# Kernel tuning notes

Hardware: AMD Instinct MI355X
Metric: run time of the kernel (lower is better)

Reference implementation:

```python
import jax, jax.numpy as jnp
import numpy as np

V, D, H, L, FF, NC = 32000, 512, 8, 4, 2048, 10
HD = D // H
EPS = 1e-5


def _layernorm(x, g, b):
    m = jnp.mean(x, axis=-1, keepdims=True)
    v = jnp.mean((x - m) ** 2, axis=-1, keepdims=True)
    return (x - m) * jax.lax.rsqrt(v + EPS) * g + b


def _pos_encoding(T, d):
    pos = jnp.arange(T, dtype=jnp.float32)[:, None]
    div = jnp.exp(jnp.arange(0, d, 2, dtype=jnp.float32) * (-np.log(10000.0) / d))
    pe = jnp.zeros((T, d), dtype=jnp.float32)
    pe = pe.at[:, 0::2].set(jnp.sin(pos * div))
    pe = pe.at[:, 1::2].set(jnp.cos(pos * div))
    return pe


def setup_inputs() -> dict:
    key = jax.random.key(0)
    ks = iter(jax.random.split(key, 32))
    n = lambda shape, s=0.02: jax.random.normal(next(ks), shape, dtype=jnp.float32) * s
    inp = {
        "tokens": jax.random.randint(next(ks), (8, 1024), 0, V),
        "emb": n((V, D), 1.0),
        # attention projections, stored (in, out) so y = x @ W + b
        "Wq": n((L, D, D)), "bq": jnp.zeros((L, D)),
        "Wk": n((L, D, D)), "bk": jnp.zeros((L, D)),
        "Wv": n((L, D, D)), "bv": jnp.zeros((L, D)),
        "Wo": n((L, D, D)), "bo": jnp.zeros((L, D)),
        "ln1_g": jnp.ones((L, D)), "ln1_b": jnp.zeros((L, D)),
        "ln2_g": jnp.ones((L, D)), "ln2_b": jnp.zeros((L, D)),
        "W1": n((L, D, FF)), "b1": jnp.zeros((L, FF)),
        "W2": n((L, FF, D)), "b2": jnp.zeros((L, D)),
        "heavy_w": n((D, D)), "heavy_b": jnp.zeros((D,)),
        "heavy_a1": n((D, D)), "heavy_a2": n((D, D)),
        "norm_g": jnp.ones((D,)), "norm_b": jnp.zeros((D,)),
        "cls_W": n((D, NC)), "cls_b": jnp.zeros((NC,)),
    }
    return inp


def reference(tokens, emb, Wq, bq, Wk, bk, Wv, bv, Wo, bo,
              ln1_g, ln1_b, ln2_g, ln2_b, W1, b1, W2, b2,
              heavy_w, heavy_b, heavy_a1, heavy_a2,
              norm_g, norm_b, cls_W, cls_b):
    B, T = tokens.shape
    x = emb[tokens] + _pos_encoding(T, D)[None]  # [B,T,D]
    scale = 1.0 / np.sqrt(HD)
    for l in range(L):
        # attention block (pre-norm)
        h = _layernorm(x, ln1_g[l], ln1_b[l])
        q = (h @ Wq[l] + bq[l]).reshape(B, T, H, HD)
        k = (h @ Wk[l] + bk[l]).reshape(B, T, H, HD)
        v = (h @ Wv[l] + bv[l]).reshape(B, T, H, HD)
        scores = jnp.einsum("bqhd,bkhd->bhqk", q, k) * scale
        attn = jax.nn.softmax(scores, axis=-1)
        o = jnp.einsum("bhqk,bkhd->bqhd", attn, v).reshape(B, T, D)
        x = x + (o @ Wo[l] + bo[l])
        # feedforward block
        h = _layernorm(x, ln2_g[l], ln2_b[l])
        x = x + (jax.nn.gelu(h @ W1[l] + b1[l], approximate=False) @ W2[l] + b2[l])
    # heavy layer: chained matmuls + bias + tanh (vectorized over B*T)
    x = jnp.tanh(((x @ heavy_w) @ heavy_a1) @ heavy_a2 + heavy_b)
    x = _layernorm(x, norm_g, norm_b)
    x = jnp.mean(x, axis=1)  # [B,D]
    return x @ cls_W + cls_b  # [B,NC]
```

## Files before the change

### kernel.cpp

```cpp
#include <hip/hip_runtime.h>
#include <math.h>

#define BS   8
#define TT   1024
#define DD   512
#define HH   8
#define LL   4
#define FFD  2048
#define NCC  10
#define MM   (BS*TT)
#define MDl  ((long)MM*DD)

typedef unsigned short u16;
typedef short  short8 __attribute__((ext_vector_type(8)));
typedef float  f32x4  __attribute__((ext_vector_type(4)));
typedef u16    u16x8  __attribute__((ext_vector_type(8)));
typedef u16    u16x4  __attribute__((ext_vector_type(4)));

static __device__ __forceinline__ u16 f2b(float f) {
    union { float f; unsigned u; } x; x.f = f;
    unsigned r = x.u + 0x7FFFu + ((x.u >> 16) & 1u);
    return (u16)(r >> 16);
}
static __device__ __forceinline__ u16 f2b_fast(float f) {
    union { float f; unsigned u; } x; x.f = f;
    return (u16)((x.u + 0x8000u) >> 16);
}
static __device__ __forceinline__ float b2f(u16 u) {
    union { unsigned u; float f; } x; x.u = ((unsigned)u) << 16;
    return x.f;
}

__global__ __launch_bounds__(256)
void embed_kernel(const int* __restrict__ tok, const float* __restrict__ emb,
                  float* __restrict__ X) {
    int i = blockIdx.x * 256 + threadIdx.x;
    int d = i & (DD - 1);
    int row = i >> 9;
    int t = row & (TT - 1);
    int j = d >> 1;
    float freq = __expf((float)(2 * j) * (-9.210340371976184f / 512.0f));
    float ang = (float)t * freq;
    float pe = (d & 1) ? cosf(ang) : sinf(ang);
    X[i] = emb[(long)tok[row] * DD + d] + pe;
}

template<int OUTBF>
__global__ __launch_bounds__(256)
void ln_kernel(const float* __restrict__ in, void* __restrict__ outp,
               const float* __restrict__ g, const float* __restrict__ b) {
    int row = blockIdx.x;
    int tid = threadIdx.x;
    const float* x = in + (long)row * DD;
    float x1 = x[tid], x2 = x[tid + 256];
    __shared__ float red[256], red2[256];
    red[tid] = x1 + x2;
    red2[tid] = x1 * x1 + x2 * x2;
    __syncthreads();
    for (int st = 128; st > 0; st >>= 1) {
        if (tid < st) { red[tid] += red[tid + st]; red2[tid] += red2[tid + st]; }
        __syncthreads();
    }
    float mean = red[0] * (1.0f / DD);
    float var = red2[0] * (1.0f / DD) - mean * mean;
    float rstd = rsqrtf(var + 1e-5f);
    float y1 = (x1 - mean) * rstd * g[tid] + b[tid];
    float y2 = (x2 - mean) * rstd * g[tid + 256] + b[tid + 256];
    if (OUTBF) {
        u16* o = (u16*)outp + (long)row * DD;
        o[tid] = f2b(y1); o[tid + 256] = f2b(y2);
    } else {
        float* o = (float*)outp + (long)row * DD;
        o[tid] = y1; o[tid + 256] = y2;
    }
}

template<int OUTBF, int HAS_BIAS, int ACT, int HAS_RES>
__global__ __launch_bounds__(512, 2)
void mfma_gemm(const u16* __restrict__ A, const u16* __restrict__ BT,
               const float* __restrict__ bias, const float* __restrict__ R,
               void* __restrict__ Cout, int N, int K) {
    __shared__ __align__(16) u16 lds[17408];
    u16* As = lds;
    u16* Bs = lds + 8192;
    const int tid = threadIdx.x;
    const int lane = tid & 63;
    const int w = tid >> 6;
    const int wm = w >> 1;
    const int wn = w & 1;
    const long bm = (long)blockIdx.y * 128;
    const long bn = (long)blockIdx.x * 128;

    f32x4 acc[2][4];
#pragma unroll
    for (int i = 0; i < 2; ++i)
#pragma unroll
        for (int j = 0; j < 4; ++j) acc[i][j] = {0.f, 0.f, 0.f, 0.f};

    const int srow = tid >> 2;
    const int sc0 = (tid & 3) * 2;
    const u16* Ag = A + (bm + srow) * K + sc0 * 8;
    const u16* Bg = BT + (bn + srow) * K + sc0 * 8;
    int soff[2];
#pragma unroll
    for (int j = 0; j < 2; ++j)
        soff[j] = srow * 64 + ((sc0 + j) ^ (srow & 7)) * 8;

    const int fr = lane & 15;
    const int g = lane >> 4;
    const int am0 = wm * 32 + fr;
    const int bn0 = wn * 64 + fr;
    const int sw = fr & 7;

    u16x8 sa[2][2], sb[2][2];
#pragma unroll
    for (int j = 0; j < 2; ++j) {
        sa[0][j] = *(const u16x8*)(Ag + j * 8);
        sb[0][j] = *(const u16x8*)(Bg + j * 8);
    }

    for (int k0 = 0; k0 < K; k0 += 128) {
#pragma unroll
        for (int half = 0; half < 2; ++half) {
            const int cb = half, nb = half ^ 1;
            __syncthreads();
#pragma unroll
            for (int j = 0; j < 2; ++j) {
                *(u16x8*)&As[soff[j]] = sa[cb][j];
                *(u16x8*)&Bs[soff[j]] = sb[cb][j];
            }
            const int knext = k0 + (half + 1) * 64;
            if (knext < K) {
#pragma unroll
                for (int j = 0; j < 2; ++j) {
                    sa[nb][j] = *(const u16x8*)(Ag + knext + j * 8);
                    sb[nb][j] = *(const u16x8*)(Bg + knext + j * 8);
                }
            }
            __syncthreads();
#pragma unroll
            for (int kk = 0; kk < 2; ++kk) {
                const int pos = ((kk << 2) + g) ^ sw;
                short8 af[2], bfv[4];
#pragma unroll
                for (int mi = 0; mi < 2; ++mi)
                    af[mi] = *(const short8*)&As[(am0 + mi * 16) * 64 + pos * 8];
#pragma unroll
                for (int ni = 0; ni < 4; ++ni)
                    bfv[ni] = *(const short8*)&Bs[(bn0 + ni * 16) * 64 + pos * 8];
#pragma unroll
                for (int mi = 0; mi < 2; ++mi)
#pragma unroll
                    for (int ni = 0; ni < 4; ++ni)
                        acc[mi][ni] = __builtin_amdgcn_mfma_f32_16x16x32_bf16(
                            af[mi], bfv[ni], acc[mi][ni], 0, 0, 0);
            }
        }
    }

    const int erow0 = wm * 32 + g * 4;
    const int ecol0 = wn * 64 + fr;

    if (OUTBF) {
        __syncthreads();
#pragma unroll
        for (int ni = 0; ni < 4; ++ni) {
            const long col = bn + ecol0 + ni * 16;
            float bv = 0.f;
            if (HAS_BIAS) bv = bias[col];
#pragma unroll
            for (int mi = 0; mi < 2; ++mi)
#pragma unroll
                for (int r = 0; r < 4; ++r) {
                    const int row = erow0 + mi * 16 + r;
                    float v = acc[mi][ni][r];
                    if (HAS_BIAS) v += bv;
                    if (ACT == 1) v = 0.5f * v * (1.0f + erff(v * 0.70710678118654752f));
                    if (ACT == 2) v = tanhf(v);
                    if (HAS_RES) v += R[(bm + row) * N + col];
                    lds[row * 136 + ecol0 + ni * 16] = f2b(v);
                }
        }
        __syncthreads();
        const int srow2 = tid >> 4;
        const int sch2 = tid & 15;
        u16* Cp = (u16*)Cout;
#pragma unroll
        for (int rr = 0; rr < 4; ++rr) {
            const int row = srow2 + rr * 32;
            u16x8 vv = *(const u16x8*)&lds[row * 136 + sch2 * 8];
            *(u16x8*)(Cp + (bm + row) * N + bn + sch2 * 8) = vv;
        }
    } else {
#pragma unroll
        for (int ni = 0; ni < 4; ++ni) {
            const long col = bn + ecol0 + ni * 16;
            float bv = 0.f;
            if (HAS_BIAS) bv = bias[col];
#pragma unroll
            for (int mi = 0; mi < 2; ++mi)
#pragma unroll
                for (int r = 0; r < 4; ++r) {
                    const long row = bm + erow0 + mi * 16 + r;
                    float v = acc[mi][ni][r];
                    if (HAS_BIAS) v += bv;
                    if (ACT == 1) v = 0.5f * v * (1.0f + erff(v * 0.70710678118654752f));
                    if (ACT == 2) v = tanhf(v);
                    if (HAS_RES) v += R[row * N + col];
                    ((float*)Cout)[row * N + col] = v;
                }
        }
    }
}

__global__ __launch_bounds__(256, 2)
void attn_kernel(const u16* __restrict__ QKV, u16* __restrict__ O) {
    const int qblk = blockIdx.x;
    const int h = blockIdx.y;
    const int b = blockIdx.z;
    const int tid = threadIdx.x;
    const int lane = tid & 63;
    const int w = tid >> 6;
    const int fr = lane & 15;
    const int g = lane >> 4;
    const int q8 = g * 8;

    __shared__ __align__(16) u16 Ks[64 * 64];
    __shared__ __align__(16) u16 Vt[64 * 72];
    __shared__ __align__(16) u16 Pw[4][32 * 72];

    const long rowb = (long)b * TT;
    const int wq0 = qblk * 128 + w * 32;

    short8 qf[2][2];
#pragma unroll
    for (int qt = 0; qt < 2; ++qt)
#pragma unroll
        for (int hf = 0; hf < 2; ++hf)
            qf[qt][hf] = *(const short8*)(QKV + (rowb + wq0 + qt * 16 + fr) * 1536
                                          + h * 64 + hf * 32 + q8);

    f32x4 accO[2][4];
    float lsum[2][4];
#pragma unroll
    for (int qt = 0; qt < 2; ++qt) {
#pragma unroll
        for (int nt = 0; nt < 4; ++nt) accO[qt][nt] = {0.f, 0.f, 0.f, 0.f};
#pragma unroll
        for (int r = 0; r < 4; ++r) lsum[qt][r] = 0.f;
    }

    const int skey = tid >> 2;
    const int skc = (tid & 3) * 2;
    const int koff0 = skey * 64 + ((skc ^ (skey & 7)) * 8);
    const int koff1 = skey * 64 + (((skc + 1) ^ (skey & 7)) * 8);
    const int vkp = tid & 31;
    const int vd0 = (tid >> 5) * 8;

    auto load_kv = [&](int kt_, u16x8* kr_, u16x8* vr_) {
        const long tb_ = (rowb + (long)kt_ * 64) * 1536 + h * 64;
        const u16* kp_ = QKV + tb_ + 512 + (long)skey * 1536 + skc * 8;
        kr_[0] = *(const u16x8*)kp_;
        kr_[1] = *(const u16x8*)(kp_ + 8);
        const u16* vp_ = QKV + tb_ + 1024 + (long)(vkp * 2) * 1536 + vd0;
        vr_[0] = *(const u16x8*)vp_;
        vr_[1] = *(const u16x8*)(vp_ + 1536);
    };
    auto stage = [&](u16x8* kr_, u16x8* vr_) {
        *(u16x8*)&Ks[koff0] = kr_[0];
        *(u16x8*)&Ks[koff1] = kr_[1];
        unsigned* Vt32 = (unsigned*)Vt;
#pragma unroll
        for (int j = 0; j < 8; ++j)
            Vt32[(vd0 + j) * 36 + vkp] =
                (unsigned)vr_[0][j] | ((unsigned)vr_[1][j] << 16);
    };
    auto compute = [&]() {
        f32x4 accS[2][4];
#pragma unroll
        for (int qt = 0; qt < 2; ++qt)
#pragma unroll
            for (int n = 0; n < 4; ++n) accS[qt][n] = {0.f, 0.f, 0.f, 0.f};
#pragma unroll
        for (int n = 0; n < 4; ++n)
#pragma unroll
            for (int hf = 0; hf < 2; ++hf) {
                short8 bk = *(const short8*)&Ks[(n * 16 + fr) * 64
                                                + ((((hf << 2) + g) ^ (fr & 7)) * 8)];
                accS[0][n] = __builtin_amdgcn_mfma_f32_16x16x32_bf16(qf[0][hf], bk, accS[0][n], 0, 0, 0);
                accS[1][n] = __builtin_amdgcn_mfma_f32_16x16x32_bf16(qf[1][hf], bk, accS[1][n], 0, 0, 0);
            }
#pragma unroll
        for (int qt = 0; qt < 2; ++qt)
#pragma unroll
            for (int r = 0; r < 4; ++r) {
                int prow = qt * 16 + g * 4 + r;
#pragma unroll
                for (int n = 0; n < 4; ++n) {
                    float pv = exp2f(accS[qt][n][r] * 0.18033688011112042f);
                    lsum[qt][r] += pv;
                    Pw[w][prow * 72 + n * 16 + fr] = f2b_fast(pv);
                }
            }
#pragma unroll
        for (int hf = 0; hf < 2; ++hf) {
            short8 pa0 = *(const short8*)&Pw[w][fr * 72 + hf * 32 + q8];
            short8 pa1 = *(const short8*)&Pw[w][(16 + fr) * 72 + hf * 32 + q8];
#pragma unroll
            for (int nt = 0; nt < 4; ++nt) {
                short8 bv = *(const short8*)&Vt[(nt * 16 + fr) * 72 + hf * 32 + q8];
                accO[0][nt] = __builtin_amdgcn_mfma_f32_16x16x32_bf16(pa0, bv, accO[0][nt], 0, 0, 0);
                accO[1][nt] = __builtin_amdgcn_mfma_f32_16x16x32_bf16(pa1, bv, accO[1][nt], 0, 0, 0);
            }
        }
    };

    u16x8 krA[2], vrA[2], krB[2], vrB[2];
    load_kv(0, krA, vrA);

#pragma unroll 1
    for (int kt = 0; kt < 16; kt += 2) {
        __syncthreads();
        stage(krA, vrA);
        load_kv(kt + 1, krB, vrB);
        __syncthreads();
        compute();
        __syncthreads();
        stage(krB, vrB);
        if (kt + 2 < 16) load_kv(kt + 2, krA, vrA);
        __syncthreads();
        compute();
    }

#pragma unroll
    for (int qt = 0; qt < 2; ++qt)
#pragma unroll
        for (int r = 0; r < 4; ++r) {
            float s = lsum[qt][r];
            s += __shfl_xor(s, 1, 64);
            s += __shfl_xor(s, 2, 64);
            s += __shfl_xor(s, 4, 64);
            s += __shfl_xor(s, 8, 64);
            lsum[qt][r] = 1.0f / s;
        }
#pragma unroll
    for (int qt = 0; qt < 2; ++qt)
#pragma unroll
        for (int nt = 0; nt < 4; ++nt)
#pragma unroll
            for (int r = 0; r < 4; ++r) {
                long row = rowb + wq0 + qt * 16 + g * 4 + r;
                O[row * DD + h * 64 + nt * 16 + fr] = f2b(accO[qt][nt][r] * lsum[qt][r]);
            }
}

struct WP   { const float* s; u16* d; };
struct WTbl { WP e[19]; };

__global__ __launch_bounds__(256)
void wprep512_kernel(WTbl tbl) {
    const float* src = tbl.e[blockIdx.z].s;
    u16* dst = tbl.e[blockIdx.z].d;
    int k0 = blockIdx.y * 32, n0 = blockIdx.x * 32;
    __shared__ float tile[32][33];
    int tx = threadIdx.x & 31, ty = threadIdx.x >> 5;
#pragma unroll
    for (int i = 0; i < 4; ++i)
        tile[ty + 8 * i][tx] = src[(long)(k0 + ty + 8 * i) * 512 + n0 + tx];
    __syncthreads();
#pragma unroll
    for (int i = 0; i < 4; ++i) {
        int r = ty + 8 * i;
        dst[(long)(n0 + r) * 512 + k0 + tx] = f2b(tile[tx][r]);
    }
}

__global__ __launch_bounds__(256)
void wprep_kernel(const float* __restrict__ src, u16* __restrict__ dst,
                  int K, int N, long srcLS, long dstLS) {
    int l = blockIdx.z;
    src += (long)l * srcLS;
    dst += (long)l * dstLS;
    int k0 = blockIdx.y * 32, n0 = blockIdx.x * 32;
    __shared__ float tile[32][33];
    int tx = threadIdx.x & 31, ty = threadIdx.x >> 5;
#pragma unroll
    for (int i = 0; i < 4; ++i)
        tile[ty + 8 * i][tx] = src[(long)(k0 + ty + 8 * i) * N + n0 + tx];
    __syncthreads();
#pragma unroll
    for (int i = 0; i < 4; ++i) {
        int r = ty + 8 * i;
        dst[(long)(n0 + r) * K + k0 + tx] = f2b(tile[tx][r]);
    }
}

__global__ __launch_bounds__(256)
void bprep_kernel(const float* __restrict__ bq, const float* __restrict__ bk,
                  const float* __restrict__ bv, float* __restrict__ dst) {
    int i = blockIdx.x * 256 + threadIdx.x;
    int l = i / 1536, j = i - l * 1536;
    float v = (j < 512) ? bq[l * 512 + j]
            : (j < 1024) ? bk[l * 512 + j - 512]
                         : bv[l * 512 + j - 1024];
    dst[i] = v;
}

__global__ __launch_bounds__(256)
void f2b_kernel(const float* __restrict__ in, u16* __restrict__ out, int n) {
    int i = blockIdx.x * 256 + threadIdx.x;
    if (i < n) out[i] = f2b(in[i]);
}

__global__ __launch_bounds__(256)
void zero_kernel(float* __restrict__ p, int n) {
    int i = blockIdx.x * 256 + threadIdx.x;
    if (i < n) p[i] = 0.0f;
}

__global__ __launch_bounds__(256)
void colmean_kernel(const float* __restrict__ Hn, float* __restrict__ XM) {
    int blk = blockIdx.x;
    int b = blk >> 5;
    int r0 = (blk & 31) * 32;
    int tid = threadIdx.x;
    float acc0 = 0.0f, acc1 = 0.0f;
    for (int r = 0; r < 32; ++r) {
        long off = ((long)b * TT + r0 + r) * DD + tid;
        acc0 += Hn[off];
        acc1 += Hn[off + 256];
    }
    atomicAdd(&XM[b * DD + tid], acc0);
    atomicAdd(&XM[b * DD + tid + 256], acc1);
}

__global__ __launch_bounds__(256)
void cls_kernel(const float* __restrict__ XM, const float* __restrict__ W,
                const float* __restrict__ bias, float* __restrict__ out) {
    int b = blockIdx.x;
    int tid = threadIdx.x;
    __shared__ float xm[DD];
    xm[tid] = XM[b * DD + tid] * (1.0f / TT);
    xm[tid + 256] = XM[b * DD + tid + 256] * (1.0f / TT);
    __syncthreads();
    if (tid < NCC) {
        float s = bias[tid];
        for (int d = 0; d < DD; ++d) s += xm[d] * W[d * NCC + tid];
        out[b * NCC + tid] = s;
    }
}

extern "C" void kernel_launch(void* const* d_in, const int* in_sizes, int n_in,
                              void* d_out, int out_size, void* d_ws, size_t ws_size,
                              hipStream_t stream) {
    const int*   tokens  = (const int*)d_in[0];
    const float* emb     = (const float*)d_in[1];
    const float* Wq      = (const float*)d_in[2];
    const float* bq      = (const float*)d_in[3];
    const float* Wk      = (const float*)d_in[4];
    const float* bk      = (const float*)d_in[5];
    const float* Wv      = (const float*)d_in[6];
    const float* bv      = (const float*)d_in[7];
    const float* Wo      = (const float*)d_in[8];
    const float* bo      = (const float*)d_in[9];
    const float* ln1_g   = (const float*)d_in[10];
    const float* ln1_b   = (const float*)d_in[11];
    const float* ln2_g   = (const float*)d_in[12];
    const float* ln2_b   = (const float*)d_in[13];
    const float* W1      = (const float*)d_in[14];
    const float* b1      = (const float*)d_in[15];
    const float* W2      = (const float*)d_in[16];
    const float* b2      = (const float*)d_in[17];
    const float* heavy_w = (const float*)d_in[18];
    const float* heavy_b = (const float*)d_in[19];
    const float* heavy_a1= (const float*)d_in[20];
    const float* heavy_a2= (const float*)d_in[21];
    const float* norm_g  = (const float*)d_in[22];
    const float* norm_b  = (const float*)d_in[23];
    const float* cls_W   = (const float*)d_in[24];
    const float* cls_b   = (const float*)d_in[25];
    float* out = (float*)d_out;

    char* p = (char*)d_ws;
    float* X    = (float*)p;  p += MDl * 4;
    u16*   Hh   = (u16*)p;    p += MDl * 2;
    u16*   QKVb = (u16*)p;
    u16*   FFb  = QKVb;
    u16*   T1   = QKVb;
    u16*   T2   = QKVb + MDl;
    float* LNout= (float*)QKVb;
    p += (long)MM * 1536 * 2;
    u16*   Ob   = (u16*)p;    p += MDl * 2;
    u16*   Xbf  = (u16*)p;    p += MDl * 2;
    u16*   WqkvT= (u16*)p;    p += 4L * 1536 * 512 * 2;
    u16*   WoT  = (u16*)p;    p += 4L * 512 * 512 * 2;
    u16*   W1T  = (u16*)p;    p += 4L * 2048 * 512 * 2;
    u16*   W2T  = (u16*)p;    p += 4L * 512 * 2048 * 2;
    u16*   WhT  = (u16*)p;    p += 3L * 512 * 512 * 2;
    float* bqkv = (float*)p;  p += 4L * 1536 * 4;
    float* XM   = (float*)p;  p += (long)BS * DD * 4;

    dim3 blk(256);
    dim3 blk512(512);

    WTbl tbl;
    for (int l = 0; l < 4; ++l) {
        tbl.e[l * 4 + 0] = {Wq + (long)l * 262144, WqkvT + (long)l * 786432};
        tbl.e[l * 4 + 1] = {Wk + (long)l * 262144, WqkvT + (long)l * 786432 + 262144};
        tbl.e[l * 4 + 2] = {Wv + (long)l * 262144, WqkvT + (long)l * 786432 + 524288};
        tbl.e[l * 4 + 3] = {Wo + (long)l * 262144, WoT + (long)l * 262144};
    }
    tbl.e[16] = {heavy_w,  WhT};
    tbl.e[17] = {heavy_a1, WhT + 262144};
    tbl.e[18] = {heavy_a2, WhT + 524288};
    wprep512_kernel<<<dim3(16, 16, 19), blk, 0, stream>>>(tbl);
    wprep_kernel<<<dim3(64, 16, 4), blk, 0, stream>>>(W1, W1T,  512, 2048, 1048576, 1048576);
    wprep_kernel<<<dim3(16, 64, 4), blk, 0, stream>>>(W2, W2T, 2048,  512, 1048576, 1048576);
    bprep_kernel<<<24, blk, 0, stream>>>(bq, bk, bv, bqkv);

    embed_kernel<<<MM * DD / 256, blk, 0, stream>>>(tokens, emb, X);

    dim3 gQKV(12, 64), g512(4, 64), gFF1(16, 64);

    for (int l = 0; l < LL; ++l) {
        ln_kernel<1><<<MM, blk, 0, stream>>>(X, Hh, ln1_g + l * DD, ln1_b + l * DD);
        mfma_gemm<1, 1, 0, 0><<<gQKV, blk512, 0, stream>>>(
            Hh, WqkvT + (long)l * 786432, bqkv + l * 1536, nullptr, QKVb, 1536, 512);
        attn_kernel<<<dim3(8, HH, BS), blk, 0, stream>>>(QKVb, Ob);
        mfma_gemm<0, 1, 0, 1><<<g512, blk512, 0, stream>>>(
            Ob, WoT + (long)l * 262144, bo + l * DD, X, X, 512, 512);
        ln_kernel<1><<<MM, blk, 0, stream>>>(X, Hh, ln2_g + l * DD, ln2_b + l * DD);
        mfma_gemm<1, 1, 1, 0><<<gFF1, blk512, 0, stream>>>(
            Hh, W1T + (long)l * 1048576, b1 + l * FFD, nullptr, FFb, 2048, 512);
        mfma_gemm<0, 1, 0, 1><<<g512, blk512, 0, stream>>>(
            FFb, W2T + (long)l * 1048576, b2 + l * DD, X, X, 512, 2048);
    }

    f2b_kernel<<<MM * DD / 256, blk, 0, stream>>>(X, Xbf, MM * DD);
    mfma_gemm<1, 0, 0, 0><<<g512, blk512, 0, stream>>>(Xbf, WhT,          nullptr, nullptr, T1, 512, 512);
    mfma_gemm<1, 0, 0, 0><<<g512, blk512, 0, stream>>>(T1,  WhT + 262144, nullptr, nullptr, T2, 512, 512);
    mfma_gemm<0, 1, 2, 0><<<g512, blk512, 0, stream>>>(T2,  WhT + 524288, heavy_b, nullptr, X,  512, 512);

    ln_kernel<0><<<MM, blk, 0, stream>>>(X, LNout, norm_g, norm_b);
    zero_kernel<<<(BS * DD + 255) / 256, blk, 0, stream>>>(XM, BS * DD);
    colmean_kernel<<<256, blk, 0, stream>>>(LNout, XM);
    cls_kernel<<<BS, blk, 0, stream>>>(XM, cls_W, cls_b, out);
}
```

Before: 829.5 us.

## Keep residual stream in bf16 and restructure GEMM k-loop double buffering

```diff
diff --git a/kernel.cpp b/kernel.cpp
--- a/kernel.cpp
+++ b/kernel.cpp
@@ -33,7 +33,7 @@
 
 __global__ __launch_bounds__(256)
 void embed_kernel(const int* __restrict__ tok, const float* __restrict__ emb,
-                  float* __restrict__ X) {
+                  u16* __restrict__ X) {
     int i = blockIdx.x * 256 + threadIdx.x;
     int d = i & (DD - 1);
     int row = i >> 9;
@@ -42,17 +42,23 @@
     float freq = __expf((float)(2 * j) * (-9.210340371976184f / 512.0f));
     float ang = (float)t * freq;
     float pe = (d & 1) ? cosf(ang) : sinf(ang);
-    X[i] = emb[(long)tok[row] * DD + d] + pe;
-}
-
-template<int OUTBF>
-__global__ __launch_bounds__(256)
-void ln_kernel(const float* __restrict__ in, void* __restrict__ outp,
+    X[i] = f2b(emb[(long)tok[row] * DD + d] + pe);
+}
+
+template<int INBF, int OUTBF>
+__global__ __launch_bounds__(256)
+void ln_kernel(const void* __restrict__ inp, void* __restrict__ outp,
                const float* __restrict__ g, const float* __restrict__ b) {
     int row = blockIdx.x;
     int tid = threadIdx.x;
-    const float* x = in + (long)row * DD;
-    float x1 = x[tid], x2 = x[tid + 256];
+    float x1, x2;
+    if (INBF) {
+        const u16* x = (const u16*)inp + (long)row * DD;
+        x1 = b2f(x[tid]); x2 = b2f(x[tid + 256]);
+    } else {
+        const float* x = (const float*)inp + (long)row * DD;
+        x1 = x[tid]; x2 = x[tid + 256];
+    }
     __shared__ float red[256], red2[256];
     red[tid] = x1 + x2;
     red2[tid] = x1 * x1 + x2 * x2;
@@ -76,13 +82,11 @@
 }
 
 template<int OUTBF, int HAS_BIAS, int ACT, int HAS_RES>
-__global__ __launch_bounds__(512, 2)
+__global__ __launch_bounds__(512, 4)
 void mfma_gemm(const u16* __restrict__ A, const u16* __restrict__ BT,
-               const float* __restrict__ bias, const float* __restrict__ R,
+               const float* __restrict__ bias, const u16* __restrict__ R,
                void* __restrict__ Cout, int N, int K) {
-    __shared__ __align__(16) u16 lds[17408];
-    u16* As = lds;
-    u16* Bs = lds + 8192;
+    __shared__ __align__(16) u16 lds[32768];
     const int tid = threadIdx.x;
     const int lane = tid & 63;
     const int w = tid >> 6;
@@ -111,50 +115,62 @@
     const int am0 = wm * 32 + fr;
     const int bn0 = wn * 64 + fr;
     const int sw = fr & 7;
-
-    u16x8 sa[2][2], sb[2][2];
+    const int nt = K >> 6;
+
+    u16x8 sa[2], sb[2];
 #pragma unroll
     for (int j = 0; j < 2; ++j) {
-        sa[0][j] = *(const u16x8*)(Ag + j * 8);
-        sb[0][j] = *(const u16x8*)(Bg + j * 8);
-    }
-
-    for (int k0 = 0; k0 < K; k0 += 128) {
-#pragma unroll
-        for (int half = 0; half < 2; ++half) {
-            const int cb = half, nb = half ^ 1;
-            __syncthreads();
+        sa[j] = *(const u16x8*)(Ag + j * 8);
+        sb[j] = *(const u16x8*)(Bg + j * 8);
+    }
+#pragma unroll
+    for (int j = 0; j < 2; ++j) {
+        *(u16x8*)&lds[soff[j]] = sa[j];
+        *(u16x8*)&lds[16384 + soff[j]] = sb[j];
+    }
+#pragma unroll
+    for (int j = 0; j < 2; ++j) {
+        sa[j] = *(const u16x8*)(Ag + 64 + j * 8);
+        sb[j] = *(const u16x8*)(Bg + 64 + j * 8);
+    }
+
+#pragma unroll 1
+    for (int i = 0; i < nt; ++i) {
+        __syncthreads();
+        const int cb = i & 1;
+        if (i + 1 < nt) {
+            const int nbase = (1 - cb) * 8192;
 #pragma unroll
             for (int j = 0; j < 2; ++j) {
-                *(u16x8*)&As[soff[j]] = sa[cb][j];
-                *(u16x8*)&Bs[soff[j]] = sb[cb][j];
+                *(u16x8*)&lds[nbase + soff[j]] = sa[j];
+                *(u16x8*)&lds[16384 + nbase + soff[j]] = sb[j];
             }
-            const int knext = k0 + (half + 1) * 64;
-            if (knext < K) {
+            if (i + 2 < nt) {
+                const int koff = (i + 2) * 64;
 #pragma unroll
                 for (int j = 0; j < 2; ++j) {
-                    sa[nb][j] = *(const u16x8*)(Ag + knext + j * 8);
-                    sb[nb][j] = *(const u16x8*)(Bg + knext + j * 8);
+                    sa[j] = *(const u16x8*)(Ag + koff + j * 8);
+                    sb[j] = *(const u16x8*)(Bg + koff + j * 8);
                 }
             }
-            __syncthreads();
-#pragma unroll
-            for (int kk = 0; kk < 2; ++kk) {
-                const int pos = ((kk << 2) + g) ^ sw;
-                short8 af[2], bfv[4];
-#pragma unroll
-                for (int mi = 0; mi < 2; ++mi)
-                    af[mi] = *(const short8*)&As[(am0 + mi * 16) * 64 + pos * 8];
+        }
+        const int cbase = cb * 8192;
+#pragma unroll
+        for (int kk = 0; kk < 2; ++kk) {
+            const int pos = ((kk << 2) + g) ^ sw;
+            short8 af[2], bfv[4];
+#pragma unroll
+            for (int mi = 0; mi < 2; ++mi)
+                af[mi] = *(const short8*)&lds[cbase + (am0 + mi * 16) * 64 + pos * 8];
+#pragma unroll
+            for (int ni = 0; ni < 4; ++ni)
+                bfv[ni] = *(const short8*)&lds[16384 + cbase + (bn0 + ni * 16) * 64 + pos * 8];
+#pragma unroll
+            for (int mi = 0; mi < 2; ++mi)
 #pragma unroll
                 for (int ni = 0; ni < 4; ++ni)
-                    bfv[ni] = *(const short8*)&Bs[(bn0 + ni * 16) * 64 + pos * 8];
-#pragma unroll
-                for (int mi = 0; mi < 2; ++mi)
-#pragma unroll
-                    for (int ni = 0; ni < 4; ++ni)
-                        acc[mi][ni] = __builtin_amdgcn_mfma_f32_16x16x32_bf16(
-                            af[mi], bfv[ni], acc[mi][ni], 0, 0, 0);
-            }
+                    acc[mi][ni] = __builtin_amdgcn_mfma_f32_16x16x32_bf16(
+                        af[mi], bfv[ni], acc[mi][ni], 0, 0, 0);
         }
     }
 
@@ -177,7 +193,7 @@
                     if (HAS_BIAS) v += bv;
                     if (ACT == 1) v = 0.5f * v * (1.0f + erff(v * 0.70710678118654752f));
                     if (ACT == 2) v = tanhf(v);
-                    if (HAS_RES) v += R[(bm + row) * N + col];
+                    if (HAS_RES) v += b2f(R[(bm + row) * N + col]);
                     lds[row * 136 + ecol0 + ni * 16] = f2b(v);
                 }
         }
@@ -206,7 +222,7 @@
                     if (HAS_BIAS) v += bv;
                     if (ACT == 1) v = 0.5f * v * (1.0f + erff(v * 0.70710678118654752f));
                     if (ACT == 2) v = tanhf(v);
-                    if (HAS_RES) v += R[row * N + col];
+                    if (HAS_RES) v += b2f(R[row * N + col]);
                     ((float*)Cout)[row * N + col] = v;
                 }
         }
@@ -407,19 +423,13 @@
 }
 
 __global__ __launch_bounds__(256)
-void f2b_kernel(const float* __restrict__ in, u16* __restrict__ out, int n) {
-    int i = blockIdx.x * 256 + threadIdx.x;
-    if (i < n) out[i] = f2b(in[i]);
-}
-
-__global__ __launch_bounds__(256)
 void zero_kernel(float* __restrict__ p, int n) {
     int i = blockIdx.x * 256 + threadIdx.x;
     if (i < n) p[i] = 0.0f;
 }
 
 __global__ __launch_bounds__(256)
-void colmean_kernel(const float* __restrict__ Hn, float* __restrict__ XM) {
+void colmean_kernel(const u16* __restrict__ Hn, float* __restrict__ XM) {
     int blk = blockIdx.x;
     int b = blk >> 5;
     int r0 = (blk & 31) * 32;
@@ -427,8 +437,8 @@
     float acc0 = 0.0f, acc1 = 0.0f;
     for (int r = 0; r < 32; ++r) {
         long off = ((long)b * TT + r0 + r) * DD + tid;
-        acc0 += Hn[off];
-        acc1 += Hn[off + 256];
+        acc0 += b2f(Hn[off]);
+        acc1 += b2f(Hn[off + 256]);
     }
     atomicAdd(&XM[b * DD + tid], acc0);
     atomicAdd(&XM[b * DD + tid + 256], acc1);
@@ -482,16 +492,14 @@
     float* out = (float*)d_out;
 
     char* p = (char*)d_ws;
-    float* X    = (float*)p;  p += MDl * 4;
+    u16*   X    = (u16*)p;    p += MDl * 2;
     u16*   Hh   = (u16*)p;    p += MDl * 2;
     u16*   QKVb = (u16*)p;
     u16*   FFb  = QKVb;
-    u16*   T1   = QKVb;
-    u16*   T2   = QKVb + MDl;
-    float* LNout= (float*)QKVb;
+    float* XF   = (float*)QKVb;
     p += (long)MM * 1536 * 2;
     u16*   Ob   = (u16*)p;    p += MDl * 2;
-    u16*   Xbf  = (u16*)p;    p += MDl * 2;
+    u16*   SCR  = (u16*)p;    p += MDl * 2;
     u16*   WqkvT= (u16*)p;    p += 4L * 1536 * 512 * 2;
     u16*   WoT  = (u16*)p;    p += 4L * 512 * 512 * 2;
     u16*   W1T  = (u16*)p;    p += 4L * 2048 * 512 * 2;
@@ -523,26 +531,25 @@
     dim3 gQKV(12, 64), g512(4, 64), gFF1(16, 64);
 
     for (int l = 0; l < LL; ++l) {
-        ln_kernel<1><<<MM, blk, 0, stream>>>(X, Hh, ln1_g + l * DD, ln1_b + l * DD);
+        ln_kernel<1, 1><<<MM, blk, 0, stream>>>(X, Hh, ln1_g + l * DD, ln1_b + l * DD);
         mfma_gemm<1, 1, 0, 0><<<gQKV, blk512, 0, stream>>>(
             Hh, WqkvT + (long)l * 786432, bqkv + l * 1536, nullptr, QKVb, 1536, 512);
         attn_kernel<<<dim3(8, HH, BS), blk, 0, stream>>>(QKVb, Ob);
-        mfma_gemm<0, 1, 0, 1><<<g512, blk512, 0, stream>>>(
+        mfma_gemm<1, 1, 0, 1><<<g512, blk512, 0, stream>>>(
             Ob, WoT + (long)l * 262144, bo + l * DD, X, X, 512, 512);
-        ln_kernel<1><<<MM, blk, 0, stream>>>(X, Hh, ln2_g + l * DD, ln2_b + l * DD);
+        ln_kernel<1, 1><<<MM, blk, 0, stream>>>(X, Hh, ln2_g + l * DD, ln2_b + l * DD);
         mfma_gemm<1, 1, 1, 0><<<gFF1, blk512, 0, stream>>>(
             Hh, W1T + (long)l * 1048576, b1 + l * FFD, nullptr, FFb, 2048, 512);
-        mfma_gemm<0, 1, 0, 1><<<g512, blk512, 0, stream>>>(
+        mfma_gemm<1, 1, 0, 1><<<g512, blk512, 0, stream>>>(
             FFb, W2T + (long)l * 1048576, b2 + l * DD, X, X, 512, 2048);
     }
 
-    f2b_kernel<<<MM * DD / 256, blk, 0, stream>>>(X, Xbf, MM * DD);
-    mfma_gemm<1, 0, 0, 0><<<g512, blk512, 0, stream>>>(Xbf, WhT,          nullptr, nullptr, T1, 512, 512);
-    mfma_gemm<1, 0, 0, 0><<<g512, blk512, 0, stream>>>(T1,  WhT + 262144, nullptr, nullptr, T2, 512, 512);
-    mfma_gemm<0, 1, 2, 0><<<g512, blk512, 0, stream>>>(T2,  WhT + 524288, heavy_b, nullptr, X,  512, 512);
-
-    ln_kernel<0><<<MM, blk, 0, stream>>>(X, LNout, norm_g, norm_b);
+    mfma_gemm<1, 0, 0, 0><<<g512, blk512, 0, stream>>>(X,   WhT,          nullptr, nullptr, Hh,  512, 512);
+    mfma_gemm<1, 0, 0, 0><<<g512, blk512, 0, stream>>>(Hh,  WhT + 262144, nullptr, nullptr, SCR, 512, 512);
+    mfma_gemm<0, 1, 2, 0><<<g512, blk512, 0, stream>>>(SCR, WhT + 524288, heavy_b, nullptr, XF,  512, 512);
+
+    ln_kernel<0, 1><<<MM, blk, 0, stream>>>(XF, Hh, norm_g, norm_b);
     zero_kernel<<<(BS * DD + 255) / 256, blk, 0, stream>>>(XM, BS * DD);
-    colmean_kernel<<<256, blk, 0, stream>>>(LNout, XM);
+    colmean_kernel<<<256, blk, 0, stream>>>(Hh, XM);
     cls_kernel<<<BS, blk, 0, stream>>>(XM, cls_W, cls_b, out);
 }
```

Measured after the change: 853.6 us. 1.03x slower.
